# Kernel optimization log

Measured on AMD Instinct MI355X. Metric: run time of the kernel, lower is better.

The kernel has to match this reference:

```python
import jax, jax.numpy as jnp
import numpy as np
import math

N_RAYS = 16384
HIDDEN = 32
Z_BOUNDS = (0.1, 1.0, 10.0)
STEPS_FIRST = (128, 64)
N_IMPORTANCE = 128
ALPHA_IMP = 0.02
INNER, OUTER = 1.0, 2.0


def _uniform_z_log():
    # get_uniform_z_vals: per-segment log10 linspace, endpoint excluded like torch code
    segs = []
    for i in range(len(STEPS_FIRST)):
        lo, hi = math.log10(Z_BOUNDS[i]), math.log10(Z_BOUNDS[i + 1])
        segs.append(np.linspace(lo, hi - (hi - lo) / STEPS_FIRST[i], STEPS_FIRST[i], dtype=np.float32))
    return jnp.asarray(np.concatenate(segs))


def _density(x, Wd1, bd1, Wd2, bd2):
    hfeat = jax.nn.relu(x @ Wd1 + bd1)            # [N,S,HIDDEN]
    sigma = jax.nn.softplus(hfeat @ Wd2 + bd2)[..., 0]  # [N,S]
    return sigma, hfeat


def _mip_scale(x):
    # mipnerf360_scale with translation_center = 0
    dist = jnp.linalg.norm(x, axis=-1, keepdims=True)
    scale = jnp.where(dist > INNER, (OUTER - (OUTER - INNER) / dist) / dist, 1.0)
    return x * scale


def _sample_points(rays_o, rays_d, z_vals):
    pts = rays_o[:, None, :] + rays_d[:, None, :] * z_vals[..., None]  # [N,S,3]
    dirs = rays_d / jnp.linalg.norm(rays_d, axis=-1, keepdims=True)
    return pts, jnp.broadcast_to(dirs[:, None, :], pts.shape)


def _weights_from_sigma(sigmas, z_log):
    # render_rays_log compositing: delta[:, -1] = 0
    delta = jnp.concatenate([z_log[:, 1:] - z_log[:, :-1], jnp.zeros_like(z_log[:, :1])], axis=-1)
    alpha = 1.0 - jnp.exp(-sigmas * delta)
    alpha_shift = jnp.concatenate([jnp.zeros_like(alpha[:, :1]), alpha[:, :-1]], axis=-1)
    weights = alpha * jnp.cumprod(1.0 - alpha_shift, axis=-1)
    return weights


def _reweight(weights):
    z = jnp.zeros_like(weights[:, :1])
    wp = jnp.concatenate([z, weights, z], axis=-1)
    w = 0.5 * (jnp.maximum(wp[:, :-2], wp[:, 1:-1]) + jnp.maximum(wp[:, 1:-1], wp[:, 2:]))
    w = w + ALPHA_IMP / w.shape[-1]
    total = sum(STEPS_FIRST)
    seg_scale = jnp.concatenate([jnp.full((s,), s / total, w.dtype) for s in STEPS_FIRST])
    w = w * seg_scale
    return w / jnp.sum(w, axis=-1, keepdims=True)


def _sample_pdf(z_vals, weights, key):
    n_rays = z_vals.shape[0]
    cdf = jnp.cumsum(weights, axis=-1)
    z_mid = 0.5 * (z_vals[:, :-1] + z_vals[:, 1:])
    u = jnp.linspace(0.0, 1.0 - 1.0 / N_IMPORTANCE, N_IMPORTANCE, dtype=z_vals.dtype)
    u = u[None, :] + jax.random.uniform(key, (n_rays, N_IMPORTANCE), dtype=z_vals.dtype) / N_IMPORTANCE
    u = u * (cdf[:, -2:-1] - cdf[:, 1:2]) + cdf[:, 1:2]
    inds = jax.vmap(lambda c, uu: jnp.searchsorted(c, uu, side='right'))(cdf[:, 1:-2], u) + 1
    g = lambda arr, idx: jnp.take_along_axis(arr, idx, axis=1)
    cdf_b, cdf_a = g(cdf, inds - 1), g(cdf, inds)
    t = (u - cdf_b) / (cdf_a - cdf_b)
    zb, za = g(z_mid, inds - 1), g(z_mid, inds)
    return zb + (za - zb) * t


def _forward(n, h, w, K, E, bg_color, Wd1, bd1, Wd2, bd2, Wc1, bc1, Wc2, bc2):
    # get_rays
    dirs = jnp.stack([w + 0.5, h + 0.5, jnp.ones_like(w)], axis=-1)        # [N,3]
    cam_dirs = dirs @ jnp.linalg.inv(K).T
    rays_d = jnp.einsum('nij,nj->ni', E[:, :3, :3], cam_dirs)
    rays_o = E[:, :3, -1]
    # efficient_sampling (no-grad coarse pass)
    n_rays = rays_o.shape[0]
    z_log_c = jnp.broadcast_to(_uniform_z_log()[None, :], (n_rays, sum(STEPS_FIRST)))
    z_c = jnp.power(10.0, z_log_c)
    xyz_c, _ = _sample_points(rays_o, rays_d, z_c)
    sig_c, _ = _density(_mip_scale(xyz_c), Wd1, bd1, Wd2, bd2)
    w_c = _weights_from_sigma(sig_c, z_log_c)
    w_re = _reweight(w_c)
    z_log_f = jax.lax.stop_gradient(_sample_pdf(z_log_c, w_re, jax.random.key(42)))
    z_f = jnp.power(10.0, z_log_f)
    # fine pass through model
    xyz, dirs_f = _sample_points(rays_o, rays_d, z_f)
    sigma, hfeat = _density(_mip_scale(xyz), Wd1, bd1, Wd2, bd2)
    feat = jnp.concatenate([hfeat, dirs_f], axis=-1)
    rgbs = jax.nn.sigmoid(jax.nn.relu(feat @ Wc1 + bc1) @ Wc2 + bc2)       # [N,S,3]
    weights = _weights_from_sigma(sigma, z_log_f)
    image = jnp.sum(weights[..., None] * rgbs, axis=-2)
    invdepth = jnp.sum(weights / z_f, axis=-1)
    image = image + (1.0 - jnp.sum(weights, axis=-1, keepdims=True)) * bg_color
    lo, hi = math.log10(Z_BOUNDS[0]), math.log10(Z_BOUNDS[-1])
    z_log_s = (z_log_f - lo) / (hi - lo)
    return image, weights, z_log_s, invdepth


def setup_inputs() -> dict:
    key = jax.random.key(0)
    ks = jax.random.split(key, 12)
    N = N_RAYS
    h = jax.random.uniform(ks[0], (N,), dtype=jnp.float32) * 1080.0
    w = jax.random.uniform(ks[1], (N,), dtype=jnp.float32) * 1920.0
    f = 1000.0
    K = jnp.array([[f, 0.0, 960.0], [0.0, f, 540.0], [0.0, 0.0, 1.0]], jnp.float32)
    t = jax.random.normal(ks[2], (N, 3), dtype=jnp.float32) * 0.1
    E = jnp.tile(jnp.eye(4, dtype=jnp.float32)[None], (N, 1, 1)).at[:, :3, 3].set(t)
    n = jax.random.randint(ks[3], (N,), 0, 100)
    bg_color = jax.random.uniform(ks[4], (3,), dtype=jnp.float32)
    Wd1 = jax.random.normal(ks[5], (3, HIDDEN), dtype=jnp.float32) * 0.5
    bd1 = jnp.zeros((HIDDEN,), jnp.float32)
    Wd2 = jax.random.normal(ks[6], (HIDDEN, 1), dtype=jnp.float32) * 0.3
    bd2 = jnp.zeros((1,), jnp.float32)
    Wc1 = jax.random.normal(ks[7], (HIDDEN + 3, HIDDEN), dtype=jnp.float32) * 0.3
    bc1 = jnp.zeros((HIDDEN,), jnp.float32)
    Wc2 = jax.random.normal(ks[8], (HIDDEN, 3), dtype=jnp.float32) * 0.3
    bc2 = jnp.zeros((3,), jnp.float32)
    return {"n": n, "h": h, "w": w, "K": K, "E": E, "bg_color": bg_color,
            "Wd1": Wd1, "bd1": bd1, "Wd2": Wd2, "bd2": bd2,
            "Wc1": Wc1, "bc1": bc1, "Wc2": Wc2, "bc2": bc2}


def reference(n, h, w, K, E, bg_color, Wd1, bd1, Wd2, bd2, Wc1, bc1, Wc2, bc2):
    return _forward(n, h, w, K, E, bg_color, Wd1, bd1, Wd2, bd2, Wc1, bc1, Wc2, bc2)
```

## Files before the change

kernel.cpp:

```cpp
#include <hip/hip_runtime.h>
#include <stdint.h>

#define SC 192
#define SF 128
#define NT 128

#define WD1   0
#define BD1   96
#define WD2   128
#define BD2   160
#define BC2   161
#define NV4   164
#define W24   292
#define SWTOT 420

#define WS_FRAG_OFF 2048
#define WS_NEED     4096

#define HSTRIDE 40
#define RGBS 4

using half8 = __attribute__((ext_vector_type(8))) _Float16;
using f32x4 = __attribute__((ext_vector_type(4))) float;

__device__ __forceinline__ float zlog_c(int t) {
  return (t < 128) ? (-1.0f + (float)t * 0.0078125f)
                   : ((float)(t - 128) * 0.015625f);
}
__device__ __forceinline__ float delta_c(int t) {
  if (t >= SC - 1) return 0.0f;
  return zlog_c(t + 1) - zlog_c(t);
}

__device__ __forceinline__ float fast_rcp(float x) { return __builtin_amdgcn_rcpf(x); }
__device__ __forceinline__ float fast_rsq(float x) { return __builtin_amdgcn_rsqf(x); }
__device__ __forceinline__ float exp10_f(float x) { return __expf(x * 2.30258509299f); }
__device__ __forceinline__ float softplus_f(float x) {
  return fmaxf(x, 0.0f) + __logf(1.0f + __expf(-fabsf(x)));
}

__device__ __forceinline__ uint32_t pk2h(float a, float b) {
  auto p = __builtin_amdgcn_cvt_pkrtz(a, b);
  uint32_t u; __builtin_memcpy(&u, &p, 4); return u;
}
__device__ __forceinline__ unsigned short f2h(float f) {
  _Float16 h = (_Float16)f;
  unsigned short us; __builtin_memcpy(&us, &h, 2); return us;
}

__device__ __forceinline__ float4 ldsf4(const float* p) { return *(const float4*)p; }

__device__ __forceinline__ void threefry2x32_k42(uint32_t& x0, uint32_t& x1) {
  const uint32_t ks0 = 0u, ks1 = 42u;
  const uint32_t ks2 = ks0 ^ ks1 ^ 0x1BD11BDAu;
  const uint32_t ks[3] = {ks0, ks1, ks2};
  const int rot[2][4] = {{13, 15, 26, 6}, {17, 29, 16, 24}};
  x0 += ks[0];
  x1 += ks[1];
#pragma unroll
  for (int i = 0; i < 5; ++i) {
#pragma unroll
    for (int j = 0; j < 4; ++j) {
      x0 += x1;
      const int r = rot[i & 1][j];
      x1 = (x1 << r) | (x1 >> (32 - r));
      x1 ^= x0;
    }
    x0 += ks[(i + 1) % 3];
    x1 += ks[(i + 2) % 3] + (uint32_t)(i + 1);
  }
}

__device__ __forceinline__ float wave_scan_mul(float v, int lane) {
#pragma unroll
  for (int d = 1; d < 64; d <<= 1) {
    float o = __shfl_up(v, d, 64);
    if (lane >= d) v *= o;
  }
  return v;
}
__device__ __forceinline__ float wave_scan_add(float v, int lane) {
#pragma unroll
  for (int d = 1; d < 64; d <<= 1) {
    float o = __shfl_up(v, d, 64);
    if (lane >= d) v += o;
  }
  return v;
}

__global__ __launch_bounds__(NT) void pack_weights(
    const float* __restrict__ Wd1, const float* __restrict__ bd1,
    const float* __restrict__ Wd2, const float* __restrict__ bd2,
    const float* __restrict__ Wc1, const float* __restrict__ bc1,
    const float* __restrict__ Wc2, const float* __restrict__ bc2,
    float* __restrict__ wsf) {
  const int t = threadIdx.x;
  for (int i = t; i < 96; i += NT) wsf[WD1 + i] = Wd1[i];
  for (int i = t; i < 32; i += NT) { wsf[BD1 + i] = bd1[i]; wsf[WD2 + i] = Wd2[i]; }
  if (t == 0) {
    wsf[BD2] = bd2[0];
    wsf[BC2 + 0] = bc2[0]; wsf[BC2 + 1] = bc2[1]; wsf[BC2 + 2] = bc2[2];
  }
  if (t < 32) {
    wsf[NV4 + t * 4 + 0] = bc1[t];
    wsf[NV4 + t * 4 + 1] = Wc1[32 * 32 + t];
    wsf[NV4 + t * 4 + 2] = Wc1[33 * 32 + t];
    wsf[NV4 + t * 4 + 3] = Wc1[34 * 32 + t];
  }
  if (t < 12) {
    const int m = t % 3, q = t / 3;
    uint32_t hw[4];
#pragma unroll
    for (int j2 = 0; j2 < 4; ++j2) {
      const int k0 = q * 8 + j2 * 2;
      hw[j2] = (uint32_t)f2h(Wc2[k0 * 3 + m])
             | ((uint32_t)f2h(Wc2[(k0 + 1) * 3 + m]) << 16);
    }
    ((uint4*)(wsf + W24))[t] = make_uint4(hw[0], hw[1], hw[2], hw[3]);
  }
  if (t < 64) {
    const int q_s = t >> 4;
    uint4* frag = (uint4*)((char*)wsf + WS_FRAG_OFF);
#pragma unroll
    for (int nt = 0; nt < 2; ++nt) {
      const int n_s = nt * 16 + (t & 15);
      uint32_t hw[4];
#pragma unroll
      for (int j2 = 0; j2 < 4; ++j2) {
        const int k = q_s * 8 + j2 * 2;
        hw[j2] = (uint32_t)f2h(Wc1[k * 32 + n_s])
               | ((uint32_t)f2h(Wc1[(k + 1) * 32 + n_s]) << 16);
      }
      frag[t * 2 + nt] = make_uint4(hw[0], hw[1], hw[2], hw[3]);
    }
  }
}

template <bool USE_WS>
__global__ __launch_bounds__(NT) void nerf_fwd(
    const float* __restrict__ hh, const float* __restrict__ ww,
    const float* __restrict__ K, const float* __restrict__ E,
    const float* __restrict__ bg,
    const float* __restrict__ Wd1, const float* __restrict__ bd1,
    const float* __restrict__ Wd2, const float* __restrict__ bd2,
    const float* __restrict__ Wc1, const float* __restrict__ bc1,
    const float* __restrict__ Wc2, const float* __restrict__ bc2,
    const float* __restrict__ wsf,
    float* __restrict__ out, int n_rays) {
  const int ray = blockIdx.x;
  const int t = threadIdx.x;
  const int lane = t & 63;
  const int wv = t >> 6;
  const int quad = lane >> 4;

  __shared__ __align__(16) float sw[SWTOT];
  __shared__ __align__(16) float s_A[32];
  __shared__ __align__(16) float s_B[32];
  __shared__ __align__(16) unsigned char u_buf[SF * HSTRIDE * 2];
  float* const s_w   = (float*)u_buf;
  float* const s_cdf = (float*)(u_buf + 768);
  unsigned short* const s_hf = (unsigned short*)u_buf;
  __shared__ float s_rgb[SF * RGBS];
  __shared__ float s_zlf[SF];
  __shared__ float s_tot[8];
  __shared__ float s_red[16];
  float* const s_dv = sw;

  if constexpr (USE_WS) {
    const float4* wsrc = (const float4*)wsf;
    float4* sdst = (float4*)sw;
    for (int i = t; i < SWTOT / 4; i += NT) sdst[i] = wsrc[i];
  } else {
    for (int i = t; i < 96; i += NT) sw[WD1 + i] = Wd1[i];
    for (int i = t; i < 32; i += NT) { sw[BD1 + i] = bd1[i]; sw[WD2 + i] = Wd2[i]; }
    if (t == 0) {
      sw[BD2] = bd2[0];
      sw[BC2 + 0] = bc2[0]; sw[BC2 + 1] = bc2[1]; sw[BC2 + 2] = bc2[2];
    }
    if (t < 32) {
      sw[NV4 + t * 4 + 0] = bc1[t];
      sw[NV4 + t * 4 + 1] = Wc1[32 * 32 + t];
      sw[NV4 + t * 4 + 2] = Wc1[33 * 32 + t];
      sw[NV4 + t * 4 + 3] = Wc1[34 * 32 + t];
    }
    if (t < 12) {
      const int m = t % 3, q = t / 3;
      uint32_t hw[4];
#pragma unroll
      for (int j2 = 0; j2 < 4; ++j2) {
        const int k0 = q * 8 + j2 * 2;
        hw[j2] = (uint32_t)f2h(Wc2[k0 * 3 + m])
               | ((uint32_t)f2h(Wc2[(k0 + 1) * 3 + m]) << 16);
      }
      ((uint4*)(sw + W24))[t] = make_uint4(hw[0], hw[1], hw[2], hw[3]);
    }
  }

  const float k00 = K[0], k01 = K[1], k02 = K[2];
  const float k10 = K[3], k11 = K[4], k12 = K[5];
  const float k20 = K[6], k21 = K[7], k22 = K[8];
  const float det = k00 * (k11 * k22 - k12 * k21)
                  - k01 * (k10 * k22 - k12 * k20)
                  + k02 * (k10 * k21 - k11 * k20);
  const float id = 1.0f / det;
  const float i00 =  (k11 * k22 - k12 * k21) * id;
  const float i01 = -(k01 * k22 - k02 * k21) * id;
  const float i02 =  (k01 * k12 - k02 * k11) * id;
  const float i10 = -(k10 * k22 - k12 * k20) * id;
  const float i11 =  (k00 * k22 - k02 * k20) * id;
  const float i12 = -(k00 * k12 - k02 * k10) * id;
  const float i20 =  (k10 * k21 - k11 * k20) * id;
  const float i21 = -(k00 * k21 - k01 * k20) * id;
  const float i22 =  (k00 * k11 - k01 * k10) * id;

  const float dwx = ww[ray] + 0.5f;
  const float dwy = hh[ray] + 0.5f;
  const float cx = i00 * dwx + i01 * dwy + i02;
  const float cy = i10 * dwx + i11 * dwy + i12;
  const float cz = i20 * dwx + i21 * dwy + i22;
  const float* Er = E + (size_t)ray * 16;
  const float ox = Er[3], oy = Er[7], oz = Er[11];
  const float dx = Er[0] * cx + Er[1] * cy + Er[2] * cz;
  const float dy = Er[4] * cx + Er[5] * cy + Er[6] * cz;
  const float dz = Er[8] * cx + Er[9] * cy + Er[10] * cz;
  const float dd = dx * dx + dy * dy + dz * dz;
  const float inv_nrm = fast_rsq(dd);
  const float ndx = dx * inv_nrm, ndy = dy * inv_nrm, ndz = dz * inv_nrm;
  const float oo  = ox * ox + oy * oy + oz * oz;
  const float od2 = 2.0f * (ox * dx + oy * dy + oz * dz);

  if (t < 32) {
    const float w0 = Wd1[t], w1 = Wd1[32 + t], w2 = Wd1[64 + t];
    s_A[t] = ox * w0 + oy * w1 + oz * w2;
    s_B[t] = dx * w0 + dy * w1 + dz * w2;
  }

  __syncthreads();

  if (t < 32) {
    const float4 nv = ldsf4(sw + NV4 + t * 4);
    s_dv[t] = nv.x + ndx * nv.y + ndy * nv.z + ndz * nv.w;
  }

  const float bd2v = sw[BD2];
  float a0, v0, a1e = 0.0f, v1e = 1.0f;
  {
    float ms0, msz0, ms1 = 0.f, msz1 = 0.f;
    {
      const float z = exp10_f(zlog_c(t));
      const float d2 = fmaf(z, fmaf(z, dd, od2), oo);
      const float r = fast_rsq(fmaxf(d2, 1.0f));
      ms0 = (2.0f - r) * r;
      msz0 = ms0 * z;
    }
    if (wv == 0) {
      const float z = exp10_f((float)t * 0.015625f);
      const float d2 = fmaf(z, fmaf(z, dd, od2), oo);
      const float r = fast_rsq(fmaxf(d2, 1.0f));
      ms1 = (2.0f - r) * r;
      msz1 = ms1 * z;
    }
    float acc0 = bd2v, acc1 = bd2v;
    if (wv == 0) {
#pragma unroll 2
      for (int c = 0; c < 8; ++c) {
        const int k4 = c * 4;
        const float4 A  = ldsf4(s_A + k4);
        const float4 B  = ldsf4(s_B + k4);
        const float4 b  = ldsf4(sw + BD1 + k4);
        const float4 wd = ldsf4(sw + WD2 + k4);
        float v;
        v = fmaf(msz0, B.x, fmaf(ms0, A.x, b.x)); acc0 += fmaxf(v, 0.0f) * wd.x;
        v = fmaf(msz0, B.y, fmaf(ms0, A.y, b.y)); acc0 += fmaxf(v, 0.0f) * wd.y;
        v = fmaf(msz0, B.z, fmaf(ms0, A.z, b.z)); acc0 += fmaxf(v, 0.0f) * wd.z;
        v = fmaf(msz0, B.w, fmaf(ms0, A.w, b.w)); acc0 += fmaxf(v, 0.0f) * wd.w;
        v = fmaf(msz1, B.x, fmaf(ms1, A.x, b.x)); acc1 += fmaxf(v, 0.0f) * wd.x;
        v = fmaf(msz1, B.y, fmaf(ms1, A.y, b.y)); acc1 += fmaxf(v, 0.0f) * wd.y;
        v = fmaf(msz1, B.z, fmaf(ms1, A.z, b.z)); acc1 += fmaxf(v, 0.0f) * wd.z;
        v = fmaf(msz1, B.w, fmaf(ms1, A.w, b.w)); acc1 += fmaxf(v, 0.0f) * wd.w;
      }
    } else {
#pragma unroll 2
      for (int c = 0; c < 8; ++c) {
        const int k4 = c * 4;
        const float4 A  = ldsf4(s_A + k4);
        const float4 B  = ldsf4(s_B + k4);
        const float4 b  = ldsf4(sw + BD1 + k4);
        const float4 wd = ldsf4(sw + WD2 + k4);
        float v;
        v = fmaf(msz0, B.x, fmaf(ms0, A.x, b.x)); acc0 += fmaxf(v, 0.0f) * wd.x;
        v = fmaf(msz0, B.y, fmaf(ms0, A.y, b.y)); acc0 += fmaxf(v, 0.0f) * wd.y;
        v = fmaf(msz0, B.z, fmaf(ms0, A.z, b.z)); acc0 += fmaxf(v, 0.0f) * wd.z;
        v = fmaf(msz0, B.w, fmaf(ms0, A.w, b.w)); acc0 += fmaxf(v, 0.0f) * wd.w;
      }
    }
    v0 = __expf(-softplus_f(acc0) * delta_c(t));
    a0 = 1.0f - v0;
    if (wv == 0) {
      v1e = __expf(-softplus_f(acc1) * delta_c(128 + t));
      a1e = 1.0f - v1e;
    }
  }

  float i0 = wave_scan_mul(v0, lane);
  float i1 = 1.0f;
  if (wv == 0) i1 = wave_scan_mul(v1e, lane);
  if (lane == 63) s_tot[wv] = i0;
  if (wv == 0 && lane == 63) s_tot[2] = i1;
  __syncthreads();
  {
    const float preC1 = s_tot[0];
    const float preC2 = s_tot[0] * s_tot[1];
    float e0x = __shfl_up(i0, 1, 64); if (lane == 0) e0x = 1.0f;
    s_w[t] = a0 * e0x * (wv ? preC1 : 1.0f);
    if (wv == 0) {
      float e1x = __shfl_up(i1, 1, 64); if (lane == 0) e1x = 1.0f;
      s_w[128 + t] = a1e * e1x * preC2;
    }
  }
  __syncthreads();

  float wre0, wre1 = 0.0f;
  {
    const float wm = (t > 0) ? s_w[t - 1] : 0.0f;
    const float w0 = s_w[t];
    const float wp = s_w[t + 1];
    wre0 = 0.5f * (fmaxf(wm, w0) + fmaxf(w0, wp)) + (0.02f / 192.0f);
    wre0 *= (t < 128) ? (128.0f / 192.0f) : (64.0f / 192.0f);
  }
  if (wv == 0) {
    const int e = 128 + t;
    const float wm = s_w[e - 1];
    const float w0 = s_w[e];
    const float wp = (e < SC - 1) ? s_w[e + 1] : 0.0f;
    wre1 = 0.5f * (fmaxf(wm, w0) + fmaxf(w0, wp)) + (0.02f / 192.0f);
    wre1 *= (64.0f / 192.0f);
  }

  float s0 = wave_scan_add(wre0, lane);
  float s1 = 0.0f;
  if (wv == 0) s1 = wave_scan_add(wre1, lane);
  if (lane == 63) s_tot[4 + wv] = s0;
  if (wv == 0 && lane == 63) s_tot[6] = s1;
  __syncthreads();
  {
    const float T0 = s_tot[4], T1 = s_tot[5], T2 = s_tot[6];
    const float inv_total = fast_rcp(T0 + T1 + T2);
    s_cdf[t] = (s0 + (wv ? T0 : 0.0f)) * inv_total;
    if (wv == 0) s_cdf[128 + t] = (s1 + T0 + T1) * inv_total;
  }
  __syncthreads();

  float zlf, zf;
  {
    const uint32_t total = (uint32_t)n_rays * 128u;
    const uint32_t halfc = total >> 1;
    const uint32_t j = (uint32_t)ray * 128u + (uint32_t)t;
    uint32_t x0, x1;
    const bool first = (j < halfc);
    if (first) { x0 = j; x1 = j + halfc; } else { x0 = j - halfc; x1 = j; }
    threefry2x32_k42(x0, x1);
    const uint32_t bits = first ? x0 : x1;
    const float fr = __uint_as_float((bits >> 9) | 0x3f800000u) - 1.0f;

    float u = (float)t * 0.0078125f + fr * 0.0078125f;
    u = u * (s_cdf[190] - s_cdf[1]) + s_cdf[1];

    int lo = 0, hi = 189;
    while (lo < hi) {
      const int mid = (lo + hi) >> 1;
      if (s_cdf[1 + mid] <= u) lo = mid + 1; else hi = mid;
    }
    const int inds = lo + 1;
    const float cb = s_cdf[inds - 1], ca = s_cdf[inds];
    const float tt = (u - cb) * fast_rcp(ca - cb);
    const float zb = 0.5f * (zlog_c(inds - 1) + zlog_c(inds));
    const float za = 0.5f * (zlog_c(inds) + zlog_c(inds + 1));
    zlf = zb + (za - zb) * tt;
    s_zlf[t] = zlf;
    zf = exp10_f(zlf);
  }
  __syncthreads();

  half8 Whi0, Whi1;
  if constexpr (USE_WS) {
    const uint4* frag = (const uint4*)((const char*)wsf + WS_FRAG_OFF);
    uint4 q0 = frag[lane * 2 + 0];
    uint4 q1 = frag[lane * 2 + 1];
    __builtin_memcpy(&Whi0, &q0, 16);
    __builtin_memcpy(&Whi1, &q1, 16);
  } else {
#pragma unroll
    for (int nt = 0; nt < 2; ++nt) {
      const int n_s = nt * 16 + (lane & 15);
      uint32_t hw[4];
#pragma unroll
      for (int j2 = 0; j2 < 4; ++j2) {
        const int k = quad * 8 + j2 * 2;
        hw[j2] = (uint32_t)f2h(Wc1[k * 32 + n_s])
               | ((uint32_t)f2h(Wc1[(k + 1) * 32 + n_s]) << 16);
      }
      uint4 q = make_uint4(hw[0], hw[1], hw[2], hw[3]);
      if (nt == 0) __builtin_memcpy(&Whi0, &q, 16);
      else         __builtin_memcpy(&Whi1, &q, 16);
    }
  }

  float sigf;
  {
    const float d2 = fmaf(zf, fmaf(zf, dd, od2), oo);
    const float r = fast_rsq(fmaxf(d2, 1.0f));
    const float msf = (2.0f - r) * r;
    const float mszf = msf * zf;
    float sig_acc = bd2v;
    uint4 tmp;
#pragma unroll
    for (int c = 0; c < 8; ++c) {
      const int k4 = c * 4;
      const float4 A  = ldsf4(s_A + k4);
      const float4 B  = ldsf4(s_B + k4);
      const float4 b  = ldsf4(sw + BD1 + k4);
      const float4 wd = ldsf4(sw + WD2 + k4);
      float h0 = fmaxf(fmaf(mszf, B.x, fmaf(msf, A.x, b.x)), 0.0f);
      float h1 = fmaxf(fmaf(mszf, B.y, fmaf(msf, A.y, b.y)), 0.0f);
      float h2 = fmaxf(fmaf(mszf, B.z, fmaf(msf, A.z, b.z)), 0.0f);
      float h3 = fmaxf(fmaf(mszf, B.w, fmaf(msf, A.w, b.w)), 0.0f);
      sig_acc += h0 * wd.x + h1 * wd.y + h2 * wd.z + h3 * wd.w;
      const uint32_t pA = pk2h(h0, h1), pB = pk2h(h2, h3);
      if ((c & 1) == 0) { tmp.x = pA; tmp.y = pB; }
      else {
        tmp.z = pA; tmp.w = pB;
        *(uint4*)(s_hf + t * HSTRIDE + (c >> 1) * 8) = tmp;
      }
    }
    sigf = softplus_f(sig_acc);
  }
  __syncthreads();

  {
    const float4 dv0 = ldsf4(s_dv + quad * 4);
    const float4 dv1 = ldsf4(s_dv + 16 + quad * 4);
    const int m15 = lane & 15;
    uint4 qf = ((const uint4*)(sw + W24))[quad * 3 + (m15 < 3 ? m15 : 0)];
    if (m15 >= 3) qf = make_uint4(0u, 0u, 0u, 0u);
    half8 W2f; __builtin_memcpy(&W2f, &qf, 16);
    const float bc2x = sw[BC2 + 0], bc2y = sw[BC2 + 1], bc2z = sw[BC2 + 2];

#pragma unroll
    for (int mt = 0; mt < 4; ++mt) {
      const int sbase = wv * 64 + mt * 16;
      const int srow = sbase + m15;
      const half8 Hf = *(const half8*)(s_hf + srow * HSTRIDE + quad * 8);

      f32x4 acc0 = {0.f, 0.f, 0.f, 0.f}, acc1 = {0.f, 0.f, 0.f, 0.f};
      acc0 = __builtin_amdgcn_mfma_f32_16x16x32_f16(Whi0, Hf, acc0, 0, 0, 0);
      acc1 = __builtin_amdgcn_mfma_f32_16x16x32_f16(Whi1, Hf, acc1, 0, 0, 0);

      uint32_t w0[2], w1[2];
      w0[0] = pk2h(fmaxf(acc0[0] + dv0.x, 0.0f), fmaxf(acc0[1] + dv0.y, 0.0f));
      w0[1] = pk2h(fmaxf(acc0[2] + dv0.z, 0.0f), fmaxf(acc0[3] + dv0.w, 0.0f));
      w1[0] = pk2h(fmaxf(acc1[0] + dv1.x, 0.0f), fmaxf(acc1[1] + dv1.y, 0.0f));
      w1[1] = pk2h(fmaxf(acc1[2] + dv1.z, 0.0f), fmaxf(acc1[3] + dv1.w, 0.0f));
      __builtin_memcpy(s_hf + srow * HSTRIDE + quad * 4, w0, 8);
      __builtin_memcpy(s_hf + srow * HSTRIDE + 16 + quad * 4, w1, 8);
    }

#pragma unroll
    for (int g = 0; g < 4; ++g) {
      const int scol = wv * 64 + g * 16 + m15;
      half8 Bav;
      __builtin_memcpy(&Bav, s_hf + scol * HSTRIDE + quad * 8, 16);
      f32x4 acc2 = {0.f, 0.f, 0.f, 0.f};
      acc2 = __builtin_amdgcn_mfma_f32_16x16x32_f16(W2f, Bav, acc2, 0, 0, 0);
      if (quad == 0) {
        float4 px;
        px.x = fast_rcp(1.0f + __expf(-(acc2[0] + bc2x)));
        px.y = fast_rcp(1.0f + __expf(-(acc2[1] + bc2y)));
        px.z = fast_rcp(1.0f + __expf(-(acc2[2] + bc2z)));
        px.w = 0.0f;
        *(float4*)(s_rgb + scol * RGBS) = px;
      }
    }
  }

  const float deltaf = (t < SF - 1) ? (s_zlf[t + 1] - zlf) : 0.0f;
  const float vf = __expf(-sigf * deltaf);
  const float af = 1.0f - vf;
  float fi = wave_scan_mul(vf, lane);
  if (lane == 63) s_tot[wv] = fi;
  __syncthreads();
  float efx = __shfl_up(fi, 1, 64); if (lane == 0) efx = 1.0f;
  const float wf = af * efx * (wv ? s_tot[0] : 1.0f);

  float* o_img = out;
  float* o_w   = out + (size_t)n_rays * 3;
  float* o_z   = out + (size_t)n_rays * (3 + 128);
  float* o_inv = out + (size_t)n_rays * (3 + 256);

  o_w[(size_t)ray * 128 + t] = wf;
  o_z[(size_t)ray * 128 + t] = (zlf + 1.0f) * 0.5f;

  const float4 rgbv = ldsf4(s_rgb + t * RGBS);
  float r0 = wf * rgbv.x;
  float r1 = wf * rgbv.y;
  float r2 = wf * rgbv.z;
  float r3 = wf, r4 = wf * fast_rcp(zf);
#pragma unroll
  for (int d = 32; d > 0; d >>= 1) {
    r0 += __shfl_down(r0, d, 64);
    r1 += __shfl_down(r1, d, 64);
    r2 += __shfl_down(r2, d, 64);
    r3 += __shfl_down(r3, d, 64);
    r4 += __shfl_down(r4, d, 64);
  }
  if (lane == 0) {
    float* p = &s_red[wv * 5];
    p[0] = r0; p[1] = r1; p[2] = r2; p[3] = r3; p[4] = r4;
  }
  __syncthreads();
  if (t == 0) {
    const float accw = s_red[3] + s_red[8];
    const float bgw = 1.0f - accw;
    o_img[(size_t)ray * 3 + 0] = (s_red[0] + s_red[5]) + bgw * bg[0];
    o_img[(size_t)ray * 3 + 1] = (s_red[1] + s_red[6]) + bgw * bg[1];
    o_img[(size_t)ray * 3 + 2] = (s_red[2] + s_red[7]) + bgw * bg[2];
    o_inv[ray] = s_red[4] + s_red[9];
  }
}

extern "C" void kernel_launch(void* const* d_in, const int* in_sizes, int n_in,
                              void* d_out, int out_size, void* d_ws, size_t ws_size,
                              hipStream_t stream) {
  const float* h   = (const float*)d_in[1];
  const float* w   = (const float*)d_in[2];
  const float* K   = (const float*)d_in[3];
  const float* E   = (const float*)d_in[4];
  const float* bg  = (const float*)d_in[5];
  const float* Wd1 = (const float*)d_in[6];
  const float* bd1 = (const float*)d_in[7];
  const float* Wd2 = (const float*)d_in[8];
  const float* bd2 = (const float*)d_in[9];
  const float* Wc1 = (const float*)d_in[10];
  const float* bc1 = (const float*)d_in[11];
  const float* Wc2 = (const float*)d_in[12];
  const float* bc2 = (const float*)d_in[13];
  const int n_rays = in_sizes[1];
  float* wsf = (float*)d_ws;

  if (ws_size >= WS_NEED) {
    pack_weights<<<1, NT, 0, stream>>>(Wd1, bd1, Wd2, bd2, Wc1, bc1, Wc2, bc2, wsf);
    nerf_fwd<true><<<n_rays, NT, 0, stream>>>(h, w, K, E, bg, Wd1, bd1, Wd2, bd2,
                                              Wc1, bc1, Wc2, bc2, wsf,
                                              (float*)d_out, n_rays);
  } else {
    nerf_fwd<false><<<n_rays, NT, 0, stream>>>(h, w, K, E, bg, Wd1, bd1, Wd2, bd2,
                                               Wc1, bc1, Wc2, bc2, nullptr,
                                               (float*)d_out, n_rays);
  }
}
```

Before: 78.66 us.

## Permute Wc1 columns so MFMA output feeds next MFMA directly in registers

Reorders the hidden-unit columns of the first color-layer weight fragment so each lane's two MFMA accumulators hold eight consecutive hidden features. Those values then form the B operand of the second color MFMA directly in registers, which removes the LDS write/read round trip. A block-wide barrier before the color stage is also dropped, since each wave reads only its own rows of s_hf. This relies on the permutation matching the MFMA input layout exactly and on no cross-wave dependency remaining at that point.

```diff
diff --git a/kernel.cpp b/kernel.cpp
--- a/kernel.cpp
+++ b/kernel.cpp
@@ -49,6 +49,10 @@
 }
 
 __device__ __forceinline__ float4 ldsf4(const float* p) { return *(const float4*)p; }
+
+__device__ __forceinline__ int hperm(int i, int ntf) {
+  return 8 * (i >> 2) + (i & 3) + ntf * 4;
+}
 
 __device__ __forceinline__ void threefry2x32_k42(uint32_t& x0, uint32_t& x1) {
   const uint32_t ks0 = 0u, ks1 = 42u;
@@ -120,10 +124,11 @@
   }
   if (t < 64) {
     const int q_s = t >> 4;
+    const int i = t & 15;
     uint4* frag = (uint4*)((char*)wsf + WS_FRAG_OFF);
 #pragma unroll
     for (int nt = 0; nt < 2; ++nt) {
-      const int n_s = nt * 16 + (t & 15);
+      const int n_s = hperm(i, nt);
       uint32_t hw[4];
 #pragma unroll
       for (int j2 = 0; j2 < 4; ++j2) {
@@ -392,7 +397,7 @@
   } else {
 #pragma unroll
     for (int nt = 0; nt < 2; ++nt) {
-      const int n_s = nt * 16 + (lane & 15);
+      const int n_s = hperm(lane & 15, nt);
       uint32_t hw[4];
 #pragma unroll
       for (int j2 = 0; j2 < 4; ++j2) {
@@ -435,11 +440,10 @@
     }
     sigf = softplus_f(sig_acc);
   }
-  __syncthreads();
-
-  {
-    const float4 dv0 = ldsf4(s_dv + quad * 4);
-    const float4 dv1 = ldsf4(s_dv + 16 + quad * 4);
+
+  {
+    const float4 dv0 = ldsf4(s_dv + quad * 8);
+    const float4 dv1 = ldsf4(s_dv + quad * 8 + 4);
     const int m15 = lane & 15;
     uint4 qf = ((const uint4*)(sw + W24))[quad * 3 + (m15 < 3 ? m15 : 0)];
     if (m15 >= 3) qf = make_uint4(0u, 0u, 0u, 0u);
@@ -448,28 +452,20 @@
 
 #pragma unroll
     for (int mt = 0; mt < 4; ++mt) {
-      const int sbase = wv * 64 + mt * 16;
-      const int srow = sbase + m15;
-      const half8 Hf = *(const half8*)(s_hf + srow * HSTRIDE + quad * 8);
+      const int scol = wv * 64 + mt * 16 + m15;
+      const half8 Hf = *(const half8*)(s_hf + scol * HSTRIDE + quad * 8);
 
       f32x4 acc0 = {0.f, 0.f, 0.f, 0.f}, acc1 = {0.f, 0.f, 0.f, 0.f};
       acc0 = __builtin_amdgcn_mfma_f32_16x16x32_f16(Whi0, Hf, acc0, 0, 0, 0);
       acc1 = __builtin_amdgcn_mfma_f32_16x16x32_f16(Whi1, Hf, acc1, 0, 0, 0);
 
-      uint32_t w0[2], w1[2];
-      w0[0] = pk2h(fmaxf(acc0[0] + dv0.x, 0.0f), fmaxf(acc0[1] + dv0.y, 0.0f));
-      w0[1] = pk2h(fmaxf(acc0[2] + dv0.z, 0.0f), fmaxf(acc0[3] + dv0.w, 0.0f));
-      w1[0] = pk2h(fmaxf(acc1[0] + dv1.x, 0.0f), fmaxf(acc1[1] + dv1.y, 0.0f));
-      w1[1] = pk2h(fmaxf(acc1[2] + dv1.z, 0.0f), fmaxf(acc1[3] + dv1.w, 0.0f));
-      __builtin_memcpy(s_hf + srow * HSTRIDE + quad * 4, w0, 8);
-      __builtin_memcpy(s_hf + srow * HSTRIDE + 16 + quad * 4, w1, 8);
-    }
-
-#pragma unroll
-    for (int g = 0; g < 4; ++g) {
-      const int scol = wv * 64 + g * 16 + m15;
-      half8 Bav;
-      __builtin_memcpy(&Bav, s_hf + scol * HSTRIDE + quad * 8, 16);
+      uint4 bw;
+      bw.x = pk2h(fmaxf(acc0[0] + dv0.x, 0.0f), fmaxf(acc0[1] + dv0.y, 0.0f));
+      bw.y = pk2h(fmaxf(acc0[2] + dv0.z, 0.0f), fmaxf(acc0[3] + dv0.w, 0.0f));
+      bw.z = pk2h(fmaxf(acc1[0] + dv1.x, 0.0f), fmaxf(acc1[1] + dv1.y, 0.0f));
+      bw.w = pk2h(fmaxf(acc1[2] + dv1.z, 0.0f), fmaxf(acc1[3] + dv1.w, 0.0f));
+      half8 Bav; __builtin_memcpy(&Bav, &bw, 16);
+
       f32x4 acc2 = {0.f, 0.f, 0.f, 0.f};
       acc2 = __builtin_amdgcn_mfma_f32_16x16x32_f16(W2f, Bav, acc2, 0, 0, 0);
       if (quad == 0) {
```

After: 80.54 us. +2.4%, slower.
